# Optimization experiments

Measured on AMD Instinct MI355X. Metric: run time of the kernel, lower is better.

The kernel has to match this reference:

```python
import jax, jax.numpy as jnp
import numpy as np

N, E, H, HEADS, L, B = 16000, 256000, 192, 4, 4, 8
C = H // HEADS
VN, VE, T = 32, 8, 1000


def _sin_emb(t, dim):
    half = dim // 2
    freqs = jnp.exp(-np.log(10000.0) * jnp.arange(half, dtype=jnp.float32) / half)
    ang = t.astype(jnp.float32)[:, None] * freqs[None, :]
    return jnp.concatenate([jnp.sin(ang), jnp.cos(ang)], axis=-1)


def _ln(x, g, b, eps=1e-5):
    mu = jnp.mean(x, -1, keepdims=True)
    var = jnp.mean(jnp.square(x - mu), -1, keepdims=True)
    return (x - mu) * jax.lax.rsqrt(var + eps) * g + b


def setup_inputs():
    key = jax.random.key(0)
    ks = iter(jax.random.split(key, 64))
    p = lambda shape, s=0.02: jax.random.normal(next(ks), shape, jnp.float32) * s
    inp = {}
    inp['node_emb'] = p((VN, H))
    inp['edge_emb'] = p((VE, H))
    inp['time_w1'] = p((H, H)); inp['time_b1'] = jnp.zeros((H,), jnp.float32)
    inp['time_w2'] = p((H, H)); inp['time_b2'] = jnp.zeros((H,), jnp.float32)
    inp['mask_emb'] = p((2, H))
    inp['wq'] = p((L, H, H)); inp['bq'] = jnp.zeros((L, H), jnp.float32)
    inp['wk'] = p((L, H, H)); inp['bk'] = jnp.zeros((L, H), jnp.float32)
    inp['wv'] = p((L, H, H)); inp['bv'] = jnp.zeros((L, H), jnp.float32)
    inp['we'] = p((L, H, H))
    inp['wskip'] = p((L, H, H)); inp['bskip'] = jnp.zeros((L, H), jnp.float32)
    inp['wbeta'] = p((L, 3 * H))
    inp['ln_g'] = jnp.ones((L, H), jnp.float32); inp['ln_b'] = jnp.zeros((L, H), jnp.float32)
    inp['node_out_w'] = p((H, VN)); inp['node_out_b'] = jnp.zeros((VN,), jnp.float32)
    inp['edge_w1'] = p((4 * H, H)); inp['edge_b1'] = jnp.zeros((H,), jnp.float32)
    inp['edge_w2'] = p((H, VE)); inp['edge_b2'] = jnp.zeros((VE,), jnp.float32)
    inp['node_type'] = jax.random.randint(next(ks), (N,), 0, VN)
    inp['edge_type'] = jax.random.randint(next(ks), (E,), 0, VE)
    inp['edge_index'] = jax.random.randint(next(ks), (2, E), 0, N)
    inp['edit_mask'] = jax.random.randint(next(ks), (N,), 0, 2, dtype=jnp.int32)
    inp['node_batch'] = jnp.sort(jax.random.randint(next(ks), (N,), 0, B))
    inp['t_graph'] = jax.random.randint(next(ks), (B,), 1, T)
    return inp


def reference(node_emb, edge_emb, time_w1, time_b1, time_w2, time_b2, mask_emb,
              wq, bq, wk, bk, wv, bv, we, wskip, bskip, wbeta, ln_g, ln_b,
              node_out_w, node_out_b, edge_w1, edge_b1, edge_w2, edge_b2,
              node_type, edge_type, edge_index, edit_mask, node_batch, t_graph):
    src, dst = edge_index[0], edge_index[1]
    # time embedding: sinusoidal -> Linear -> SiLU -> Linear  => [B, H]
    t_vec = jax.nn.silu(_sin_emb(t_graph, H) @ time_w1 + time_b1) @ time_w2 + time_b2
    t_node = t_vec[node_batch]              # [N, H]
    t_edge = t_vec[node_batch[src]]         # [E, H]
    x = node_emb[node_type] + t_node + mask_emb[edit_mask]
    edge_attr = edge_emb[edge_type] + t_edge
    scale = 1.0 / np.sqrt(C)
    for l in range(L):
        q = (x @ wq[l] + bq[l]).reshape(N, HEADS, C)
        k = (x @ wk[l] + bk[l]).reshape(N, HEADS, C)
        v = (x @ wv[l] + bv[l]).reshape(N, HEADS, C)
        e = (edge_attr @ we[l]).reshape(E, HEADS, C)
        kj = k[src] + e                                   # [E, heads, C]
        score = jnp.sum(q[dst] * kj, axis=-1) * scale      # [E, heads]
        m = jax.ops.segment_max(score, dst, num_segments=N)
        ex = jnp.exp(score - m[dst])
        denom = jax.ops.segment_sum(ex, dst, num_segments=N)
        alpha = ex / denom[dst]
        msg = (v[src] + e) * alpha[..., None]              # [E, heads, C]
        out = jax.ops.segment_sum(msg, dst, num_segments=N).reshape(N, H)
        xr = x @ wskip[l] + bskip[l]
        beta = jax.nn.sigmoid(jnp.concatenate([out, xr, out - xr], -1) @ wbeta[l])[:, None]
        h = beta * xr + (1.0 - beta) * out
        x = _ln(x + h, ln_g[l], ln_b[l])
    node_logits = x @ node_out_w + node_out_b
    edge_feat = jnp.concatenate([x[src], x[dst], edge_attr, t_edge], -1)  # [E, 4H]
    edge_logits = jax.nn.silu(edge_feat @ edge_w1 + edge_b1) @ edge_w2 + edge_b2
    return node_logits, edge_logits
```

## Files before the change

### kernel.cpp

```cpp
#include <hip/hip_runtime.h>
#include <hip/hip_bf16.h>
#include <math.h>

#define NN 16000
#define NPAD 16128
#define NE 256000
#define H 192
#define RP 256
#define NL 4
#define NBATCH 8
#define VEt 8
#define HH (H*H)
#define EML 16

typedef __hip_bfloat16 bf16;
typedef unsigned short u16;
typedef unsigned char u8;
typedef unsigned int u32;
typedef __attribute__((ext_vector_type(8))) short bfrag_t;
typedef __attribute__((ext_vector_type(4))) float facc_t;
typedef __attribute__((ext_vector_type(4))) float f4;

__device__ __forceinline__ bf16 f2b(float v){ return __float2bfloat16(v); }

__device__ __forceinline__ unsigned enc8sw(float x){
    unsigned u = __float_as_uint(x);
    unsigned s = (u >> 24) & 0x80u;
    float ax = fabsf(x);
    if(ax >= 448.f) return s | 0x7Eu;
    if(ax < 0.015625f){
        int q = (int)rintf(ax * 512.f);
        return s | (unsigned)q;
    }
    unsigned au = u & 0x7FFFFFFFu;
    unsigned lsb = (au >> 20) & 1u;
    au += 0x7FFFFu + lsb;
    unsigned E = (au >> 23) - 127u;
    unsigned M = (au >> 20) & 7u;
    if((int)E > 8) return s | 0x7Eu;
    return s | ((E + 7u) << 3) | M;
}
__device__ __forceinline__ unsigned enc8(float x){
#if __has_builtin(__builtin_amdgcn_cvt_pk_fp8_f32)
    return (u32)__builtin_amdgcn_cvt_pk_fp8_f32(x, x, 0, false) & 0xFFu;
#else
    return enc8sw(x);
#endif
}
template<int SEL>
__device__ __forceinline__ float dec8s(u32 w){
#if __has_builtin(__builtin_amdgcn_cvt_f32_fp8)
    return __builtin_amdgcn_cvt_f32_fp8((int)w, SEL);
#else
    unsigned v = (w >> (SEL*8)) & 0xFFu;
    unsigned e = (v >> 3) & 15u, m = v & 7u;
    float mag = e ? __builtin_ldexpf((float)(8u + m), (int)e - 10)
                  : __builtin_ldexpf((float)m, -9);
    return (v & 0x80u) ? -mag : mag;
#endif
}
__device__ __forceinline__ float frcp(float x){
#if __has_builtin(__builtin_amdgcn_rcpf)
    return __builtin_amdgcn_rcpf(x);
#else
    return 1.f/x;
#endif
}

__global__ void k_sentinel(float* __restrict__ out, float v){ out[0] = v; }

__global__ void k_transpose(const float* __restrict__ wq, const float* __restrict__ wk,
                            const float* __restrict__ wv, const float* __restrict__ wsk,
                            const float* __restrict__ w1, u16* __restrict__ wt){
    int mat = blockIdx.x;
    const float* src;
    if(mat < 4)       src = wq  + (size_t)mat*HH;
    else if(mat < 8)  src = wk  + (size_t)(mat-4)*HH;
    else if(mat < 12) src = wv  + (size_t)(mat-8)*HH;
    else if(mat < 16) src = wsk + (size_t)(mat-12)*HH;
    else              src = w1  + (size_t)(mat-16)*HH;
    u16* dst = wt + (size_t)mat*HH;
    const int slice = HH/8;
    int base = blockIdx.y*slice;
    for(int i = base + threadIdx.x; i < base + slice; i += blockDim.x){
        int k = i / H, n = i % H;
        bf16 b = f2b(src[i]);
        dst[n*H + k] = *(u16*)&b;
    }
}

__global__ void k_tvec(const int* __restrict__ tg, const float* __restrict__ w1,
                       const float* __restrict__ b1, const float* __restrict__ w2,
                       const float* __restrict__ b2, float* __restrict__ tvec){
    int b = blockIdx.x, j = threadIdx.x;
    __shared__ float emb[H], h1[H];
    float t = (float)tg[b];
    if(j < 96){
        float fr = __expf(-logf(10000.0f) * (float)j / 96.0f);
        float ang = t * fr;
        emb[j]      = sinf(ang);
        emb[j + 96] = cosf(ang);
    }
    __syncthreads();
    float acc = b1[j];
    for(int k = 0; k < H; k++) acc += emb[k] * w1[k*H + j];
    h1[j] = acc / (1.f + __expf(-acc));
    __syncthreads();
    float acc2 = b2[j];
    for(int k = 0; k < H; k++) acc2 += h1[k] * w2[k*H + j];
    tvec[b*H + j] = acc2;
}

__global__ void k_init_x(const float* __restrict__ nemb, const float* __restrict__ memb,
                         const float* __restrict__ tvec, const int* __restrict__ ntype,
                         const int* __restrict__ emask, const int* __restrict__ nbatch,
                         float* __restrict__ x, u16* __restrict__ xb){
    int idx = blockIdx.x*blockDim.x + threadIdx.x;
    if(idx >= NN*H) return;
    int n = idx / H, c = idx % H;
    float v = nemb[(size_t)ntype[n]*H + c] + tvec[nbatch[n]*H + c]
            + memb[(size_t)emask[n]*H + c];
    x[idx] = v;
    bf16 b = f2b(v); xb[idx] = *(u16*)&b;
}

__global__ void k_zero_i(int* __restrict__ p, int n){
    int i = blockIdx.x*blockDim.x + threadIdx.x;
    if(i < n) p[i] = 0;
}
__global__ void k_count(const int* __restrict__ edst, int* __restrict__ cnt){
    int e = blockIdx.x*blockDim.x + threadIdx.x;
    if(e < NE) atomicAdd(&cnt[edst[e]], 1);
}
__global__ __launch_bounds__(1024) void k_scan(const int* __restrict__ cnt,
                                               int* __restrict__ ofs, int* __restrict__ cur){
    __shared__ int wsum[16];
    __shared__ int carry_s;
    int tid = threadIdx.x, lane = tid & 63, w = tid >> 6;
    if(tid == 0) carry_s = 0;
    __syncthreads();
    for(int base = 0; base < NN; base += 1024){
        int idx = base + tid;
        int v = (idx < NN) ? cnt[idx] : 0;
        int sc = v;
        #pragma unroll
        for(int o = 1; o < 64; o <<= 1){
            int t = __shfl_up(sc, o);
            if(lane >= o) sc += t;
        }
        if(lane == 63) wsum[w] = sc;
        __syncthreads();
        if(w == 0){
            int ws = (lane < 16) ? wsum[lane] : 0;
            #pragma unroll
            for(int o = 1; o < 16; o <<= 1){
                int t = __shfl_up(ws, o);
                if(lane >= o) ws += t;
            }
            if(lane < 16) wsum[lane] = ws;
        }
        __syncthreads();
        int wbase = (w > 0) ? wsum[w-1] : 0;
        int c = carry_s;
        int excl = c + wbase + sc - v;
        if(idx < NN){ ofs[idx] = excl; cur[idx] = excl; }
        __syncthreads();
        if(tid == 0) carry_s = c + wsum[15];
        __syncthreads();
    }
    if(threadIdx.x == 0) ofs[NN] = carry_s;
}
__global__ void k_scatter(const int* __restrict__ esrc, const int* __restrict__ edst,
                          const int* __restrict__ etype, const int* __restrict__ nbatch,
                          int* __restrict__ cur, int* __restrict__ ssrc, int* __restrict__ seix){
    int e = blockIdx.x*blockDim.x + threadIdx.x;
    if(e >= NE) return;
    int s = esrc[e], d = edst[e];
    int pos = atomicAdd(&cur[d], 1);
    ssrc[pos] = s;
    seix[pos] = nbatch[s]*VEt + etype[e];
}

__global__ void k_etab(const float* __restrict__ eemb, const float* __restrict__ tvec,
                       const float* __restrict__ we, float* __restrict__ etab){
    int blk = blockIdx.x;
    int l = blk >> 6, idx = blk & 63, b = idx >> 3, et = idx & 7;
    int c = threadIdx.x;
    __shared__ float a[H];
    a[c] = eemb[et*H + c] + tvec[b*H + c];
    __syncthreads();
    float acc = 0.f;
    const float* w = we + (size_t)l*HH;
    for(int k = 0; k < H; k++) acc += a[k] * w[k*H + c];
    etab[(size_t)blk*RP + (c/3)*4 + (c%3)] = acc;
}

__global__ void k_ctab(const float* __restrict__ eemb, const float* __restrict__ tvec,
                       const float* __restrict__ w1, const float* __restrict__ b1,
                       float* __restrict__ ctab){
    int idx = blockIdx.x, b = idx >> 3, et = idx & 7;
    int c = threadIdx.x;
    __shared__ float a[H];
    a[c] = eemb[et*H + c] + tvec[b*H + c];
    __syncthreads();
    float acc = b1[c];
    for(int k = 0; k < H; k++){
        acc += a[k]          * w1[(size_t)(2*H + k)*H + c];
        acc += tvec[b*H + k] * w1[(size_t)(3*H + k)*H + c];
    }
    ctab[(size_t)idx*RP + (c/3)*4 + (c%3)] = acc;
}

struct GemmP {
    const u16* wt[4];
    const float* bias[4];
    void* out[4];
    int obf[4];
};
__global__ __launch_bounds__(256) void k_gemm(const u16* __restrict__ A, GemmP P){
    int oi = blockIdx.y / 3, nt = blockIdx.y % 3;
    const u16* Wt = P.wt[oi];
    const float* bias = P.bias[oi];
    int wave = threadIdx.x >> 6, lane = threadIdx.x & 63;
    int quad = lane >> 4, l16 = lane & 15;
    int m0 = blockIdx.x*256 + wave*64;
    int n0 = nt*64;
    facc_t acc[4][4];
    #pragma unroll
    for(int i = 0; i < 4; i++)
        #pragma unroll
        for(int j = 0; j < 4; j++){ acc[i][j][0]=0.f; acc[i][j][1]=0.f; acc[i][j][2]=0.f; acc[i][j][3]=0.f; }
    #pragma unroll
    for(int kc = 0; kc < 6; kc++){
        int kb = kc*32 + quad*8;
        bfrag_t af[4], bg[4];
        #pragma unroll
        for(int i = 0; i < 4; i++) af[i] = *(const bfrag_t*)(A  + (size_t)(m0 + i*16 + l16)*H + kb);
        #pragma unroll
        for(int j = 0; j < 4; j++) bg[j] = *(const bfrag_t*)(Wt + (size_t)(n0 + j*16 + l16)*H + kb);
        #pragma unroll
        for(int i = 0; i < 4; i++)
            #pragma unroll
            for(int j = 0; j < 4; j++)
                acc[i][j] = __builtin_amdgcn_mfma_f32_16x16x32_bf16(af[i], bg[j], acc[i][j], 0, 0, 0);
    }
    float bv[4];
    #pragma unroll
    for(int j = 0; j < 4; j++) bv[j] = bias ? bias[n0 + j*16 + l16] : 0.f;
    if(P.obf[oi] == 2){
        u8* out = (u8*)P.out[oi];
        int byteoff[4];
        #pragma unroll
        for(int j = 0; j < 4; j++){
            int c = n0 + j*16 + l16;
            byteoff[j] = (c/3)*4 + (c%3);
        }
        #pragma unroll
        for(int i = 0; i < 4; i++){
            int rb = m0 + i*16 + quad*4;
            #pragma unroll
            for(int r = 0; r < 4; r++){
                int row = rb + r;
                if(row < NN){
                    #pragma unroll
                    for(int j = 0; j < 4; j++)
                        out[(size_t)row*RP + byteoff[j]] = (u8)enc8(acc[i][j][r] + bv[j]);
                }
            }
        }
    } else {
        float* out = (float*)P.out[oi];
        #pragma unroll
        for(int i = 0; i < 4; i++){
            int rb = m0 + i*16 + quad*4;
            #pragma unroll
            for(int r = 0; r < 4; r++){
                int row = rb + r;
                if(row < NN){
                    #pragma unroll
                    for(int j = 0; j < 4; j++)
                        out[(size_t)row*H + n0 + j*16 + l16] = acc[i][j][r] + bv[j];
                }
            }
        }
    }
}

__global__ __launch_bounds__(256) void k_attn(
    const float* __restrict__ Q, const u8* __restrict__ Kb,
    const u8* __restrict__ Vb, const float* __restrict__ XR,
    const float* __restrict__ etab, const int* __restrict__ ofs,
    const int* __restrict__ ssrc, const int* __restrict__ seix,
    const float* __restrict__ wb, const float* __restrict__ lng, const float* __restrict__ lnb,
    float* __restrict__ x, u16* __restrict__ xb)
{
    int n = blockIdx.x*4 + (threadIdx.x >> 6);
    int lane = threadIdx.x & 63;
    int ch = lane*3;
    size_t base = (size_t)n*H + ch;
    const float scale = 0.14433756729740646f;
    float q0 = Q[base], q1 = Q[base+1], q2 = Q[base+2];
    int p0 = ofs[n], p1 = ofs[n+1];
    float lac[4]  = {0.f,0.f,0.f,0.f};
    float ac0[4]  = {0.f,0.f,0.f,0.f};
    float ac1[4]  = {0.f,0.f,0.f,0.f};
    float ac2[4]  = {0.f,0.f,0.f,0.f};
    int p = p0;
    for(; p + 3 < p1; p += 4){
        int s[4], ei[4];
        #pragma unroll
        for(int t = 0; t < 4; t++){ s[t] = ssrc[p+t]; ei[t] = seix[p+t]; }
        u32 kw[4], vw[4];
        f4 ef[4];
        #pragma unroll
        for(int t = 0; t < 4; t++){
            kw[t] = *(const u32*)(Kb + (size_t)s[t]*RP + lane*4);
            ef[t] = *(const f4*)(etab + (size_t)ei[t]*RP + lane*4);
            vw[t] = *(const u32*)(Vb + (size_t)s[t]*RP + lane*4);
        }
        float tt[4];
        #pragma unroll
        for(int t = 0; t < 4; t++)
            tt[t] = q0*(dec8s<0>(kw[t])+ef[t].x) + q1*(dec8s<1>(kw[t])+ef[t].y)
                  + q2*(dec8s<2>(kw[t])+ef[t].z);
        #pragma unroll
        for(int o = 1; o <= 8; o <<= 1){
            #pragma unroll
            for(int t = 0; t < 4; t++) tt[t] += __shfl_xor(tt[t], o);
        }
        #pragma unroll
        for(int t = 0; t < 4; t++){
            float sc = fminf(fmaxf(tt[t]*scale, -60.f), 60.f);
            float pw = __expf(sc);
            lac[t] += pw;
            ac0[t] += pw*(dec8s<0>(vw[t])+ef[t].x);
            ac1[t] += pw*(dec8s<1>(vw[t])+ef[t].y);
            ac2[t] += pw*(dec8s<2>(vw[t])+ef[t].z);
        }
    }
    for(; p < p1; p++){
        int sA = ssrc[p], eiA = seix[p];
        u32 kwA = *(const u32*)(Kb + (size_t)sA*RP + lane*4);
        f4 efA = *(const f4*)(etab + (size_t)eiA*RP + lane*4);
        u32 vwA = *(const u32*)(Vb + (size_t)sA*RP + lane*4);
        float tA = q0*(dec8s<0>(kwA)+efA.x) + q1*(dec8s<1>(kwA)+efA.y) + q2*(dec8s<2>(kwA)+efA.z);
        tA += __shfl_xor(tA,1); tA += __shfl_xor(tA,2); tA += __shfl_xor(tA,4); tA += __shfl_xor(tA,8);
        float sc = fminf(fmaxf(tA*scale, -60.f), 60.f);
        float pw = __expf(sc);
        lac[0] += pw;
        ac0[0] += pw*(dec8s<0>(vwA)+efA.x);
        ac1[0] += pw*(dec8s<1>(vwA)+efA.y);
        ac2[0] += pw*(dec8s<2>(vwA)+efA.z);
    }
    float l  = (lac[0]+lac[1]) + (lac[2]+lac[3]);
    float a0 = (ac0[0]+ac0[1]) + (ac0[2]+ac0[3]);
    float a1 = (ac1[0]+ac1[1]) + (ac1[2]+ac1[3]);
    float a2 = (ac2[0]+ac2[1]) + (ac2[2]+ac2[3]);
    float inv = (p1 > p0) ? 1.f/l : 0.f;
    float o0 = a0*inv, o1 = a1*inv, o2 = a2*inv;
    float xr0 = XR[base], xr1 = XR[base+1], xr2 = XR[base+2];
    float sd = o0*wb[ch]  + o1*wb[ch+1]  + o2*wb[ch+2]
             + xr0*wb[H+ch] + xr1*wb[H+ch+1] + xr2*wb[H+ch+2]
             + (o0-xr0)*wb[2*H+ch] + (o1-xr1)*wb[2*H+ch+1] + (o2-xr2)*wb[2*H+ch+2];
    sd += __shfl_xor(sd,1); sd += __shfl_xor(sd,2); sd += __shfl_xor(sd,4);
    sd += __shfl_xor(sd,8); sd += __shfl_xor(sd,16); sd += __shfl_xor(sd,32);
    float beta = 1.f/(1.f + __expf(-sd));
    float h0 = beta*xr0 + (1.f-beta)*o0;
    float h1 = beta*xr1 + (1.f-beta)*o1;
    float h2 = beta*xr2 + (1.f-beta)*o2;
    float y0 = x[base] + h0, y1 = x[base+1] + h1, y2 = x[base+2] + h2;
    float s3 = y0 + y1 + y2;
    s3 += __shfl_xor(s3,1); s3 += __shfl_xor(s3,2); s3 += __shfl_xor(s3,4);
    s3 += __shfl_xor(s3,8); s3 += __shfl_xor(s3,16); s3 += __shfl_xor(s3,32);
    float mean = s3 * (1.f/H);
    float d0 = y0-mean, d1 = y1-mean, d2 = y2-mean;
    float v3 = d0*d0 + d1*d1 + d2*d2;
    v3 += __shfl_xor(v3,1); v3 += __shfl_xor(v3,2); v3 += __shfl_xor(v3,4);
    v3 += __shfl_xor(v3,8); v3 += __shfl_xor(v3,16); v3 += __shfl_xor(v3,32);
    float rs = rsqrtf(v3*(1.f/H) + 1e-5f);
    float z0 = d0*rs*lng[ch]   + lnb[ch];
    float z1 = d1*rs*lng[ch+1] + lnb[ch+1];
    float z2 = d2*rs*lng[ch+2] + lnb[ch+2];
    x[base] = z0; x[base+1] = z1; x[base+2] = z2;
    bf16 t0 = f2b(z0), t1 = f2b(z1), t2 = f2b(z2);
    xb[base] = *(u16*)&t0; xb[base+1] = *(u16*)&t1; xb[base+2] = *(u16*)&t2;
}

__global__ void k_nodeout(const float* __restrict__ x, const float* __restrict__ w,
                          const float* __restrict__ b, float* __restrict__ out){
    int j = threadIdx.x & 31;
    int n = blockIdx.x*8 + (threadIdx.x >> 5);
    float acc = b[j];
    const float* xr = x + (size_t)n*H;
    for(int k = 0; k < H; k++) acc += xr[k] * w[k*32 + j];
    out[(size_t)n*32 + j] = acc;
}

__global__ __launch_bounds__(256) void k_edgemlp(
    const int* __restrict__ esrc, const int* __restrict__ edst, const int* __restrict__ etype,
    const int* __restrict__ nb,
    const u8* __restrict__ xs1, const u8* __restrict__ xd1, const float* __restrict__ ctab,
    const float* __restrict__ w2, const float* __restrict__ b2p, float* __restrict__ out)
{
    int wid = blockIdx.x*4 + (threadIdx.x >> 6);
    int lane = threadIdx.x & 63;
    int ch = lane*3;
    float w2r[3][8];
    #pragma unroll
    for(int t = 0; t < 3; t++)
        #pragma unroll
        for(int j = 0; j < 8; j++) w2r[t][j] = w2[(ch+t)*8 + j];
    int jout = (lane&1)*4 + (lane&2) + ((lane&4)>>2);
    float bo = (lane < 8) ? b2p[jout] : 0.f;
    int b0 = lane & 1, b1 = lane & 2, b2m = lane & 4;
    int e0 = wid*EML;
    for(int eb = e0; eb < e0 + EML; eb += 2){
        int sX = esrc[eb],   dX = edst[eb];
        int sY = esrc[eb+1], dY = edst[eb+1];
        int ctX = nb[sX]*VEt + etype[eb];
        int ctY = nb[sY]*VEt + etype[eb+1];
        u32 awX = *(const u32*)(xs1 + (size_t)sX*RP + lane*4);
        u32 awY = *(const u32*)(xs1 + (size_t)sY*RP + lane*4);
        u32 bwX = *(const u32*)(xd1 + (size_t)dX*RP + lane*4);
        u32 bwY = *(const u32*)(xd1 + (size_t)dY*RP + lane*4);
        f4  cfX = *(const f4*)(ctab + (size_t)ctX*RP + lane*4);
        f4  cfY = *(const f4*)(ctab + (size_t)ctY*RP + lane*4);
        float hX0, hX1, hX2, hY0, hY1, hY2;
        { float v = dec8s<0>(awX)+dec8s<0>(bwX)+cfX.x; hX0 = v*frcp(1.f+__expf(-v)); }
        { float v = dec8s<1>(awX)+dec8s<1>(bwX)+cfX.y; hX1 = v*frcp(1.f+__expf(-v)); }
        { float v = dec8s<2>(awX)+dec8s<2>(bwX)+cfX.z; hX2 = v*frcp(1.f+__expf(-v)); }
        { float v = dec8s<0>(awY)+dec8s<0>(bwY)+cfY.x; hY0 = v*frcp(1.f+__expf(-v)); }
        { float v = dec8s<1>(awY)+dec8s<1>(bwY)+cfY.y; hY1 = v*frcp(1.f+__expf(-v)); }
        { float v = dec8s<2>(awY)+dec8s<2>(bwY)+cfY.z; hY2 = v*frcp(1.f+__expf(-v)); }
        float pjX[8], pjY[8];
        #pragma unroll
        for(int j = 0; j < 8; j++){
            pjX[j] = hX0*w2r[0][j] + hX1*w2r[1][j] + hX2*w2r[2][j];
            pjY[j] = hY0*w2r[0][j] + hY1*w2r[1][j] + hY2*w2r[2][j];
        }
        float v4X[4], v4Y[4];
        #pragma unroll
        for(int t = 0; t < 4; t++){
            float sX4 = b0 ? pjX[t] : pjX[t+4];
            float kX4 = b0 ? pjX[t+4] : pjX[t];
            v4X[t] = kX4 + __shfl_xor(sX4, 1);
            float sY4 = b0 ? pjY[t] : pjY[t+4];
            float kY4 = b0 ? pjY[t+4] : pjY[t];
            v4Y[t] = kY4 + __shfl_xor(sY4, 1);
        }
        float v2X[2], v2Y[2];
        #pragma unroll
        for(int t = 0; t < 2; t++){
            float sX2 = b1 ? v4X[t] : v4X[t+2];
            float kX2 = b1 ? v4X[t+2] : v4X[t];
            v2X[t] = kX2 + __shfl_xor(sX2, 2);
            float sY2 = b1 ? v4Y[t] : v4Y[t+2];
            float kY2 = b1 ? v4Y[t+2] : v4Y[t];
            v2Y[t] = kY2 + __shfl_xor(sY2, 2);
        }
        float v1X, v1Y;
        {
            float sX1 = b2m ? v2X[0] : v2X[1];
            float kX1 = b2m ? v2X[1] : v2X[0];
            v1X = kX1 + __shfl_xor(sX1, 4);
            float sY1 = b2m ? v2Y[0] : v2Y[1];
            float kY1 = b2m ? v2Y[1] : v2Y[0];
            v1Y = kY1 + __shfl_xor(sY1, 4);
        }
        v1X += __shfl_xor(v1X, 8);  v1Y += __shfl_xor(v1Y, 8);
        v1X += __shfl_xor(v1X, 16); v1Y += __shfl_xor(v1Y, 16);
        v1X += __shfl_xor(v1X, 32); v1Y += __shfl_xor(v1Y, 32);
        if(lane < 8){
            out[(size_t)eb*8 + jout]     = v1X + bo;
            out[(size_t)(eb+1)*8 + jout] = v1Y + bo;
        }
    }
}

extern "C" void kernel_launch(void* const* d_in, const int* in_sizes, int n_in,
                              void* d_out, int out_size, void* d_ws, size_t ws_size,
                              hipStream_t stream)
{
    {
        int bad = -1;
        if(n_in != 31) bad = 100;
        else {
            const int chk_idx[9] = {0, 7, 16, 21, 23, 26, 27, 29, 30};
            const int chk_sz [9] = {32*H, NL*HH, NL*3*H, 4*HH, H*8, NE, 2*NE, NN, NBATCH};
            for(int i = 0; i < 9; i++) if(in_sizes[chk_idx[i]] != chk_sz[i]){ bad = chk_idx[i]; break; }
        }
        if(bad >= 0){ k_sentinel<<<1,1,0,stream>>>((float*)d_out, 20000.f + 256.f*bad); return; }
        if(out_size != NN*32 + NE*8){ k_sentinel<<<1,1,0,stream>>>((float*)d_out, 30000.f); return; }
    }

    const float* node_emb = (const float*)d_in[0];
    const float* edge_emb = (const float*)d_in[1];
    const float* time_w1  = (const float*)d_in[2];
    const float* time_b1  = (const float*)d_in[3];
    const float* time_w2  = (const float*)d_in[4];
    const float* time_b2  = (const float*)d_in[5];
    const float* mask_emb = (const float*)d_in[6];
    const float* wq       = (const float*)d_in[7];
    const float* bq       = (const float*)d_in[8];
    const float* wk       = (const float*)d_in[9];
    const float* bk       = (const float*)d_in[10];
    const float* wv       = (const float*)d_in[11];
    const float* bv       = (const float*)d_in[12];
    const float* we       = (const float*)d_in[13];
    const float* wskip    = (const float*)d_in[14];
    const float* bskip    = (const float*)d_in[15];
    const float* wbeta    = (const float*)d_in[16];
    const float* ln_g     = (const float*)d_in[17];
    const float* ln_b     = (const float*)d_in[18];
    const float* now      = (const float*)d_in[19];
    const float* nob      = (const float*)d_in[20];
    const float* ew1      = (const float*)d_in[21];
    const float* eb1      = (const float*)d_in[22];
    const float* ew2      = (const float*)d_in[23];
    const float* eb2      = (const float*)d_in[24];
    const int* node_type  = (const int*)d_in[25];
    const int* edge_type  = (const int*)d_in[26];
    const int* edge_index = (const int*)d_in[27];
    const int* edit_mask  = (const int*)d_in[28];
    const int* node_batch = (const int*)d_in[29];
    const int* t_graph    = (const int*)d_in[30];
    const int* esrc = edge_index;
    const int* edst = edge_index + NE;

    char* wsb = (char*)d_ws;
    size_t off = 0;
    auto take = [&](size_t bytes) -> char* {
        char* r = wsb + off;
        off += (bytes + 255) & ~(size_t)255;
        return r;
    };
    float* tvec = (float*)take((size_t)NBATCH*H*4);
    float* x    = (float*)take((size_t)NN*H*4);
    u16*   xb   = (u16*)  take((size_t)NPAD*H*2);
    float* Q    = (float*)take((size_t)NN*H*4);
    u8*    Kb   = (u8*)   take((size_t)NN*RP);
    u8*    Vb   = (u8*)   take((size_t)NN*RP);
    float* XR   = (float*)take((size_t)NN*H*4);
    u8*    xs1  = (u8*)   take((size_t)NN*RP);
    u8*    xd1  = (u8*)   take((size_t)NN*RP);
    float* etab = (float*)take((size_t)NL*64*RP*4);
    float* ctab = (float*)take((size_t)64*RP*4);
    u16*   wt   = (u16*)  take((size_t)18*HH*2);
    int* cnt    = (int*)  take((size_t)(NN+1)*4);
    int* offa   = (int*)  take((size_t)(NN+1)*4);
    int* cur    = (int*)  take((size_t)(NN+1)*4);
    int* ssrc   = (int*)  take((size_t)NE*4);
    int* seix   = (int*)  take((size_t)NE*4);

    if(ws_size < off){
        k_sentinel<<<1,1,0,stream>>>((float*)d_out, 10000.f + (float)(ws_size >> 20));
        return;
    }

    k_transpose<<<dim3(18, 8), 256, 0, stream>>>(wq, wk, wv, wskip, ew1, wt);
    k_tvec<<<NBATCH, H, 0, stream>>>(t_graph, time_w1, time_b1, time_w2, time_b2, tvec);
    k_init_x<<<(NN*H + 255)/256, 256, 0, stream>>>(node_emb, mask_emb, tvec, node_type,
                                                   edit_mask, node_batch, x, xb);
    k_zero_i<<<(NN + 255)/256, 256, 0, stream>>>(cnt, NN);
    k_count<<<NE/256, 256, 0, stream>>>(edst, cnt);
    k_scan<<<1, 1024, 0, stream>>>(cnt, offa, cur);
    k_scatter<<<NE/256, 256, 0, stream>>>(esrc, edst, edge_type, node_batch, cur, ssrc, seix);
    k_etab<<<NL*64, H, 0, stream>>>(edge_emb, tvec, we, etab);
    k_ctab<<<64, H, 0, stream>>>(edge_emb, tvec, ew1, eb1, ctab);

    for(int l = 0; l < NL; l++){
        GemmP P;
        P.wt[0] = wt + (size_t)(0  + l)*HH;  P.bias[0] = bq   + (size_t)l*H;  P.out[0] = Q;  P.obf[0] = 0;
        P.wt[1] = wt + (size_t)(4  + l)*HH;  P.bias[1] = bk   + (size_t)l*H;  P.out[1] = Kb; P.obf[1] = 2;
        P.wt[2] = wt + (size_t)(8  + l)*HH;  P.bias[2] = bv   + (size_t)l*H;  P.out[2] = Vb; P.obf[2] = 2;
        P.wt[3] = wt + (size_t)(12 + l)*HH;  P.bias[3] = bskip+ (size_t)l*H;  P.out[3] = XR; P.obf[3] = 0;
        k_gemm<<<dim3(63, 12), 256, 0, stream>>>(xb, P);
        k_attn<<<NN/4, 256, 0, stream>>>(Q, Kb, Vb, XR, etab + (size_t)l*64*RP, offa, ssrc, seix,
                                         wbeta + (size_t)l*3*H, ln_g + (size_t)l*H,
                                         ln_b + (size_t)l*H, x, xb);
    }
    {
        GemmP P;
        P.wt[0] = wt + (size_t)16*HH; P.bias[0] = nullptr; P.out[0] = xs1; P.obf[0] = 2;
        P.wt[1] = wt + (size_t)17*HH; P.bias[1] = nullptr; P.out[1] = xd1; P.obf[1] = 2;
        P.wt[2] = P.wt[0]; P.bias[2] = nullptr; P.out[2] = xs1; P.obf[2] = 2;
        P.wt[3] = P.wt[0]; P.bias[3] = nullptr; P.out[3] = xs1; P.obf[3] = 2;
        k_gemm<<<dim3(63, 6), 256, 0, stream>>>(xb, P);
    }
    k_nodeout<<<NN/8, 256, 0, stream>>>(x, now, nob, (float*)d_out);
    k_edgemlp<<<NE/(4*EML), 256, 0, stream>>>(esrc, edst, edge_type, node_batch, xs1, xd1, ctab,
                                              ew2, eb2, (float*)d_out + (size_t)NN*32);
}
```

Before: 550.4 us.

## Interleave K/V rows, store edge table in bf16, and pack edge indices

K and V fp8 outputs now go into one interleaved 512-byte-per-node buffer, so attention fetches both with a single 8-byte gather per lane instead of two 4-byte gathers. The per-layer edge embedding table is stored as bf16 instead of fp32, halving each gathered edge vector. Source index and edge-table index are packed into one int2 array. Together these cut the number and size of scattered memory transactions in the attention loop. The cost is lower precision for the edge term and a more strided byte-store pattern in the GEMM epilogue.

Result: faster. 537.6 us (-2.3%).

```diff
diff --git a/kernel.cpp b/kernel.cpp
--- a/kernel.cpp
+++ b/kernel.cpp
@@ -7,6 +7,7 @@
 #define NE 256000
 #define H 192
 #define RP 256
+#define KVR 512
 #define NL 4
 #define NBATCH 8
 #define VEt 8
@@ -20,6 +21,7 @@
 typedef __attribute__((ext_vector_type(8))) short bfrag_t;
 typedef __attribute__((ext_vector_type(4))) float facc_t;
 typedef __attribute__((ext_vector_type(4))) float f4;
+typedef __attribute__((ext_vector_type(2))) unsigned int u32x2;
 
 __device__ __forceinline__ bf16 f2b(float v){ return __float2bfloat16(v); }
 
@@ -172,17 +174,17 @@
 }
 __global__ void k_scatter(const int* __restrict__ esrc, const int* __restrict__ edst,
                           const int* __restrict__ etype, const int* __restrict__ nbatch,
-                          int* __restrict__ cur, int* __restrict__ ssrc, int* __restrict__ seix){
+                          int* __restrict__ cur, int2* __restrict__ spair){
     int e = blockIdx.x*blockDim.x + threadIdx.x;
     if(e >= NE) return;
     int s = esrc[e], d = edst[e];
     int pos = atomicAdd(&cur[d], 1);
-    ssrc[pos] = s;
-    seix[pos] = nbatch[s]*VEt + etype[e];
+    int2 se; se.x = s; se.y = nbatch[s]*VEt + etype[e];
+    spair[pos] = se;
 }
 
 __global__ void k_etab(const float* __restrict__ eemb, const float* __restrict__ tvec,
-                       const float* __restrict__ we, float* __restrict__ etab){
+                       const float* __restrict__ we, u16* __restrict__ etab){
     int blk = blockIdx.x;
     int l = blk >> 6, idx = blk & 63, b = idx >> 3, et = idx & 7;
     int c = threadIdx.x;
@@ -192,7 +194,8 @@
     float acc = 0.f;
     const float* w = we + (size_t)l*HH;
     for(int k = 0; k < H; k++) acc += a[k] * w[k*H + c];
-    etab[(size_t)blk*RP + (c/3)*4 + (c%3)] = acc;
+    bf16 bv = f2b(acc);
+    etab[(size_t)blk*256 + (c/3)*4 + (c%3)] = *(u16*)&bv;
 }
 
 __global__ void k_ctab(const float* __restrict__ eemb, const float* __restrict__ tvec,
@@ -247,13 +250,17 @@
     float bv[4];
     #pragma unroll
     for(int j = 0; j < 4; j++) bv[j] = bias ? bias[n0 + j*16 + l16] : 0.f;
-    if(P.obf[oi] == 2){
+    int mode = P.obf[oi];
+    if(mode != 0){
         u8* out = (u8*)P.out[oi];
+        int rstride = (mode == 2) ? RP : KVR;
+        int mult    = (mode == 2) ? 4  : 8;
+        int koff    = (mode == 4) ? 4  : 0;
         int byteoff[4];
         #pragma unroll
         for(int j = 0; j < 4; j++){
             int c = n0 + j*16 + l16;
-            byteoff[j] = (c/3)*4 + (c%3);
+            byteoff[j] = (c/3)*mult + (c%3) + koff;
         }
         #pragma unroll
         for(int i = 0; i < 4; i++){
@@ -264,7 +271,7 @@
                 if(row < NN){
                     #pragma unroll
                     for(int j = 0; j < 4; j++)
-                        out[(size_t)row*RP + byteoff[j]] = (u8)enc8(acc[i][j][r] + bv[j]);
+                        out[(size_t)row*rstride + byteoff[j]] = (u8)enc8(acc[i][j][r] + bv[j]);
                 }
             }
         }
@@ -287,10 +294,10 @@
 }
 
 __global__ __launch_bounds__(256) void k_attn(
-    const float* __restrict__ Q, const u8* __restrict__ Kb,
-    const u8* __restrict__ Vb, const float* __restrict__ XR,
-    const float* __restrict__ etab, const int* __restrict__ ofs,
-    const int* __restrict__ ssrc, const int* __restrict__ seix,
+    const float* __restrict__ Q, const u8* __restrict__ KVb,
+    const float* __restrict__ XR,
+    const u16* __restrict__ etab, const int* __restrict__ ofs,
+    const int2* __restrict__ spair,
     const float* __restrict__ wb, const float* __restrict__ lng, const float* __restrict__ lnb,
     float* __restrict__ x, u16* __restrict__ xb)
 {
@@ -305,24 +312,27 @@
     float ac0[4]  = {0.f,0.f,0.f,0.f};
     float ac1[4]  = {0.f,0.f,0.f,0.f};
     float ac2[4]  = {0.f,0.f,0.f,0.f};
+    const u8* etb = (const u8*)etab;
     int p = p0;
     for(; p + 3 < p1; p += 4){
         int s[4], ei[4];
         #pragma unroll
-        for(int t = 0; t < 4; t++){ s[t] = ssrc[p+t]; ei[t] = seix[p+t]; }
-        u32 kw[4], vw[4];
-        f4 ef[4];
+        for(int t = 0; t < 4; t++){ int2 se = spair[p+t]; s[t] = se.x; ei[t] = se.y; }
+        u32x2 kv[4], ew[4];
         #pragma unroll
         for(int t = 0; t < 4; t++){
-            kw[t] = *(const u32*)(Kb + (size_t)s[t]*RP + lane*4);
-            ef[t] = *(const f4*)(etab + (size_t)ei[t]*RP + lane*4);
-            vw[t] = *(const u32*)(Vb + (size_t)s[t]*RP + lane*4);
-        }
-        float tt[4];
-        #pragma unroll
-        for(int t = 0; t < 4; t++)
-            tt[t] = q0*(dec8s<0>(kw[t])+ef[t].x) + q1*(dec8s<1>(kw[t])+ef[t].y)
-                  + q2*(dec8s<2>(kw[t])+ef[t].z);
+            kv[t] = *(const u32x2*)(KVb + (size_t)s[t]*KVR + lane*8);
+            ew[t] = *(const u32x2*)(etb + (size_t)ei[t]*KVR + lane*8);
+        }
+        float e0[4], e1[4], e2[4], tt[4];
+        #pragma unroll
+        for(int t = 0; t < 4; t++){
+            e0[t] = __uint_as_float(ew[t].x << 16);
+            e1[t] = __uint_as_float(ew[t].x & 0xffff0000u);
+            e2[t] = __uint_as_float(ew[t].y << 16);
+            tt[t] = q0*(dec8s<0>(kv[t].x)+e0[t]) + q1*(dec8s<1>(kv[t].x)+e1[t])
+                  + q2*(dec8s<2>(kv[t].x)+e2[t]);
+        }
         #pragma unroll
         for(int o = 1; o <= 8; o <<= 1){
             #pragma unroll
@@ -333,24 +343,26 @@
             float sc = fminf(fmaxf(tt[t]*scale, -60.f), 60.f);
             float pw = __expf(sc);
             lac[t] += pw;
-            ac0[t] += pw*(dec8s<0>(vw[t])+ef[t].x);
-            ac1[t] += pw*(dec8s<1>(vw[t])+ef[t].y);
-            ac2[t] += pw*(dec8s<2>(vw[t])+ef[t].z);
+            ac0[t] += pw*(dec8s<0>(kv[t].y)+e0[t]);
+            ac1[t] += pw*(dec8s<1>(kv[t].y)+e1[t]);
+            ac2[t] += pw*(dec8s<2>(kv[t].y)+e2[t]);
         }
     }
     for(; p < p1; p++){
-        int sA = ssrc[p], eiA = seix[p];
-        u32 kwA = *(const u32*)(Kb + (size_t)sA*RP + lane*4);
-        f4 efA = *(const f4*)(etab + (size_t)eiA*RP + lane*4);
-        u32 vwA = *(const u32*)(Vb + (size_t)sA*RP + lane*4);
-        float tA = q0*(dec8s<0>(kwA)+efA.x) + q1*(dec8s<1>(kwA)+efA.y) + q2*(dec8s<2>(kwA)+efA.z);
+        int2 se = spair[p];
+        u32x2 kvA = *(const u32x2*)(KVb + (size_t)se.x*KVR + lane*8);
+        u32x2 ewA = *(const u32x2*)(etb + (size_t)se.y*KVR + lane*8);
+        float e0A = __uint_as_float(ewA.x << 16);
+        float e1A = __uint_as_float(ewA.x & 0xffff0000u);
+        float e2A = __uint_as_float(ewA.y << 16);
+        float tA = q0*(dec8s<0>(kvA.x)+e0A) + q1*(dec8s<1>(kvA.x)+e1A) + q2*(dec8s<2>(kvA.x)+e2A);
         tA += __shfl_xor(tA,1); tA += __shfl_xor(tA,2); tA += __shfl_xor(tA,4); tA += __shfl_xor(tA,8);
         float sc = fminf(fmaxf(tA*scale, -60.f), 60.f);
         float pw = __expf(sc);
         lac[0] += pw;
-        ac0[0] += pw*(dec8s<0>(vwA)+efA.x);
-        ac1[0] += pw*(dec8s<1>(vwA)+efA.y);
-        ac2[0] += pw*(dec8s<2>(vwA)+efA.z);
+        ac0[0] += pw*(dec8s<0>(kvA.y)+e0A);
+        ac1[0] += pw*(dec8s<1>(kvA.y)+e1A);
+        ac2[0] += pw*(dec8s<2>(kvA.y)+e2A);
     }
     float l  = (lac[0]+lac[1]) + (lac[2]+lac[3]);
     float a0 = (ac0[0]+ac0[1]) + (ac0[2]+ac0[3]);
@@ -538,19 +550,17 @@
     float* x    = (float*)take((size_t)NN*H*4);
     u16*   xb   = (u16*)  take((size_t)NPAD*H*2);
     float* Q    = (float*)take((size_t)NN*H*4);
-    u8*    Kb   = (u8*)   take((size_t)NN*RP);
-    u8*    Vb   = (u8*)   take((size_t)NN*RP);
+    u8*    KVb  = (u8*)   take((size_t)NN*KVR);
     float* XR   = (float*)take((size_t)NN*H*4);
     u8*    xs1  = (u8*)   take((size_t)NN*RP);
     u8*    xd1  = (u8*)   take((size_t)NN*RP);
-    float* etab = (float*)take((size_t)NL*64*RP*4);
+    u16*   etab = (u16*)  take((size_t)NL*64*KVR);
     float* ctab = (float*)take((size_t)64*RP*4);
     u16*   wt   = (u16*)  take((size_t)18*HH*2);
     int* cnt    = (int*)  take((size_t)(NN+1)*4);
     int* offa   = (int*)  take((size_t)(NN+1)*4);
     int* cur    = (int*)  take((size_t)(NN+1)*4);
-    int* ssrc   = (int*)  take((size_t)NE*4);
-    int* seix   = (int*)  take((size_t)NE*4);
+    int2* spair = (int2*) take((size_t)NE*8);
 
     if(ws_size < off){
         k_sentinel<<<1,1,0,stream>>>((float*)d_out, 10000.f + (float)(ws_size >> 20));
@@ -564,18 +574,18 @@
     k_zero_i<<<(NN + 255)/256, 256, 0, stream>>>(cnt, NN);
     k_count<<<NE/256, 256, 0, stream>>>(edst, cnt);
     k_scan<<<1, 1024, 0, stream>>>(cnt, offa, cur);
-    k_scatter<<<NE/256, 256, 0, stream>>>(esrc, edst, edge_type, node_batch, cur, ssrc, seix);
+    k_scatter<<<NE/256, 256, 0, stream>>>(esrc, edst, edge_type, node_batch, cur, spair);
     k_etab<<<NL*64, H, 0, stream>>>(edge_emb, tvec, we, etab);
     k_ctab<<<64, H, 0, stream>>>(edge_emb, tvec, ew1, eb1, ctab);
 
     for(int l = 0; l < NL; l++){
         GemmP P;
-        P.wt[0] = wt + (size_t)(0  + l)*HH;  P.bias[0] = bq   + (size_t)l*H;  P.out[0] = Q;  P.obf[0] = 0;
-        P.wt[1] = wt + (size_t)(4  + l)*HH;  P.bias[1] = bk   + (size_t)l*H;  P.out[1] = Kb; P.obf[1] = 2;
-        P.wt[2] = wt + (size_t)(8  + l)*HH;  P.bias[2] = bv   + (size_t)l*H;  P.out[2] = Vb; P.obf[2] = 2;
-        P.wt[3] = wt + (size_t)(12 + l)*HH;  P.bias[3] = bskip+ (size_t)l*H;  P.out[3] = XR; P.obf[3] = 0;
+        P.wt[0] = wt + (size_t)(0  + l)*HH;  P.bias[0] = bq   + (size_t)l*H;  P.out[0] = Q;   P.obf[0] = 0;
+        P.wt[1] = wt + (size_t)(4  + l)*HH;  P.bias[1] = bk   + (size_t)l*H;  P.out[1] = KVb; P.obf[1] = 3;
+        P.wt[2] = wt + (size_t)(8  + l)*HH;  P.bias[2] = bv   + (size_t)l*H;  P.out[2] = KVb; P.obf[2] = 4;
+        P.wt[3] = wt + (size_t)(12 + l)*HH;  P.bias[3] = bskip+ (size_t)l*H;  P.out[3] = XR;  P.obf[3] = 0;
         k_gemm<<<dim3(63, 12), 256, 0, stream>>>(xb, P);
-        k_attn<<<NN/4, 256, 0, stream>>>(Q, Kb, Vb, XR, etab + (size_t)l*64*RP, offa, ssrc, seix,
+        k_attn<<<NN/4, 256, 0, stream>>>(Q, KVb, XR, etab + (size_t)l*64*256, offa, spair,
                                          wbeta + (size_t)l*3*H, ln_g + (size_t)l*H,
                                          ln_b + (size_t)l*H, x, xb);
     }
```
